# Performance work log

Measured on AMD Instinct MI355X. Metric: run time of the kernel, lower is better.

## Reference

```python
import jax, jax.numpy as jnp
import numpy as np

ATTRACTION_W = 1.0
REPULSION_W = 1.0
MARGIN = 0.3  # hardcoded local `margin = 0.3` in the torch forward


def setup_inputs() -> dict:
    key = jax.random.key(0)
    k1, k2, k3 = jax.random.split(key, 3)
    B, N, D, K = 16, 65536, 32, 512
    beta = jax.random.normal(k1, (B, N, 1), dtype=jnp.float32)
    embed = jax.random.normal(k2, (B, N, D), dtype=jnp.float32)
    # instance id per hit: -1 = background, 0..K-1 = instances
    sid = jax.random.randint(k3, (B, N), -1, K).astype(jnp.int32)
    # first K hits are the condensation points, one per instance
    sid = sid.at[:, :K].set(jnp.arange(K, dtype=jnp.int32)[None, :])
    is_cp = jnp.zeros((B, N), dtype=jnp.int32).at[:, :K].set(1)
    return {"beta": beta, "embed": embed, "slice_id": sid, "is_cp": is_cp, "num_instances": K}


def _per_batch(beta_b, emb_b, sid, iscp, K):
    # beta_b: [N], emb_b: [N, D], sid/iscp: [N]
    N = sid.shape[0]
    cp = iscp == 1
    valid = sid >= 0
    noncp = valid & ~cp  # non-cp signal hits
    pos = cp.sum().astype(jnp.float32)
    neg = jnp.float32(N) - pos  # noncp + background
    pos_w = jax.lax.stop_gradient(neg / (pos + 1e-6))
    w = jnp.where(cp, pos_w, jnp.where(noncp, 1.0, 2.0))
    # weighted BCE-with-logits, reduction='mean'
    x = beta_b
    y = cp.astype(jnp.float32)
    bce = jnp.maximum(x, 0.0) - x * y + jnp.log1p(jnp.exp(-jnp.abs(x)))
    beta_ce = (w * bce).mean()

    # segment id: valid hits -> sid, background -> dummy segment K (dropped)
    seg = jnp.where(valid, sid, K)
    counts = jax.ops.segment_sum(valid.astype(jnp.float32), seg, num_segments=K + 1)[:K]
    inst_exists = counts > 0  # the `unique()` set

    # first cp hit index per instance (sentinel N if instance has no cp)
    idxs = jnp.arange(N)
    first_cp = jax.ops.segment_min(jnp.where(cp & valid, idxs, N), seg, num_segments=K + 1)[:K]
    has_cp = first_cp < N
    safe_cp = jnp.minimum(first_cp, N - 1)
    cp_emb = emb_b[safe_cp]  # [K, D]
    cp_beta = beta_b[safe_cp]  # [K]

    # attraction: sum over instances (with a cp) of mean ||e_hit - e_cp||^2
    sid_c = jnp.clip(sid, 0, K - 1)
    d2 = ((emb_b - cp_emb[sid_c]) ** 2).sum(-1)  # [N]
    d2 = jnp.where(valid, d2, 0.0)
    seg_d2 = jax.ops.segment_sum(d2, seg, num_segments=K + 1)[:K]
    attr = (jnp.where(has_cp & inst_exists, seg_d2 / jnp.maximum(counts, 1.0), 0.0).sum()
            * ATTRACTION_W)

    # ranking: instances with exactly 1 cp and >0 noncp hits
    cp_count = jax.ops.segment_sum((cp & valid).astype(jnp.float32), seg, num_segments=K + 1)[:K]
    ncp_count = jax.ops.segment_sum(noncp.astype(jnp.float32), seg, num_segments=K + 1)[:K]
    r = jax.nn.relu(beta_b + MARGIN - cp_beta[sid_c])
    r = jnp.where(noncp, r, 0.0)
    seg_r = jax.ops.segment_sum(r, seg, num_segments=K + 1)[:K]
    qual = (cp_count == 1.0) & (ncp_count > 0)
    n_unique = inst_exists.sum().astype(jnp.float32)
    ranking = (jnp.where(qual, seg_r / jnp.maximum(ncp_count, 1.0), 0.0).sum()
               / jnp.maximum(n_unique, 1.0))

    beta_loss = beta_ce + 2.0 * ranking

    # repulsion over all cp hits; data has exactly one cp per instance so the
    # cp set equals cp_emb (K points), matching torch's emb_b[cp_idx]
    diff = cp_emb[:, None, :] - cp_emb[None, :, :]  # [K, K, D]
    rep = jnp.exp(-(diff ** 2).sum(-1)).mean() * REPULSION_W

    return beta_loss + attr + rep, beta_loss, attr, rep


def reference(beta, embed, slice_id, is_cp, num_instances):
    K = int(num_instances)
    beta2 = beta[..., 0]  # squeeze(-1)
    loss_b, bl, al, rl = jax.vmap(lambda b, e, s, c: _per_batch(b, e, s, c, K))(
        beta2, embed, slice_id, is_cp)
    return loss_b.mean(), bl.mean(), al.mean(), rl.mean()
```

## Files before the change

kernel.cpp:

```cpp
#include <hip/hip_runtime.h>
#include <math.h>

#define N_HITS 65536
#define K_INST 512
#define MARGIN 0.3f
#define MAXB   16
#define BPB    32
#define HITS_PB (N_HITS / BPB)

__device__ int    g_cnt[MAXB * K_INST];
__device__ float  g_d2v[MAXB * K_INST];
__device__ float  g_rv [MAXB * K_INST];
__device__ int    g_fcp[MAXB * K_INST];
__device__ float  g_cpbeta[MAXB * K_INST];
__device__ float4 g_cpemb[MAXB * K_INST * 8];
__device__ int    g_pcc[MAXB * BPB * K_INST];
__device__ float  g_pcd[MAXB * BPB * K_INST];
__device__ float  g_pcr[MAXB * BPB * K_INST];
__device__ int    g_pos[MAXB];
__device__ float  g_scp[MAXB], g_sncp[MAXB], g_sbg[MAXB];
__device__ float  g_attr[MAXB], g_rank[MAXB], g_nuq[MAXB], g_rep[MAXB];
__device__ int    g_ctr;

__global__ __launch_bounds__(256) void k_init() {
    int i = blockIdx.x * 256 + threadIdx.x;
    if (i < MAXB * K_INST) {
        g_cnt[i] = 0; g_d2v[i] = 0.f; g_rv[i] = 0.f;
        g_fcp[i] = 0x7F7F7F7F;
    }
    if (i < MAXB) {
        g_pos[i] = 0; g_scp[i] = 0.f; g_sncp[i] = 0.f; g_sbg[i] = 0.f;
        g_attr[i] = 0.f; g_rank[i] = 0.f; g_nuq[i] = 0.f; g_rep[i] = 0.f;
    }
    if (i == 0) g_ctr = 0;
}

__global__ __launch_bounds__(256) void k_scan(
    const int* __restrict__ sid, const int* __restrict__ iscp) {
    int b = blockIdx.y;
    size_t bo = (size_t)b * N_HITS;
    int i = blockIdx.x * 256 + threadIdx.x;
    int stride = gridDim.x * 256;
    for (; i < N_HITS; i += stride) {
        int c = iscp[bo + i];
        if (c == 1) {
            atomicAdd(&g_pos[b], 1);
            int s = sid[bo + i];
            if (s >= 0) atomicMin(&g_fcp[b * K_INST + s], i);
        }
    }
}

__global__ __launch_bounds__(256) void k_gather(
    const float* __restrict__ beta, const float4* __restrict__ embed4, int B) {
    int g = blockIdx.x * 256 + threadIdx.x;
    int total = B * K_INST * 8;
    if (g >= total) return;
    int row = g >> 3, sub = g & 7;
    int b = row / K_INST;
    int fc = g_fcp[row];
    int safe = min(fc, N_HITS - 1);
    float4 e = embed4[((size_t)b * N_HITS + safe) * 8 + sub];
    g_cpemb[(size_t)row * 8 + sub] = e;
    if (sub == 0) g_cpbeta[row] = beta[b * N_HITS + safe];
}

__global__ __launch_bounds__(256) void k_bce(
    const float* __restrict__ beta,
    const int* __restrict__ sid_g, const int* __restrict__ iscp_g, int B) {
    __shared__ float l_cb[K_INST];
    __shared__ int   l_cnt[K_INST];
    __shared__ float l_r[K_INST];
    __shared__ float l_red[12];

    int b = blockIdx.y, tid = threadIdx.x;
    size_t bo = (size_t)b * N_HITS;
    int base = blockIdx.x * HITS_PB;

    for (int k = tid; k < K_INST; k += 256) {
        l_cnt[k] = 0; l_r[k] = 0.f;
        l_cb[k] = g_cpbeta[b * K_INST + k];
    }
    __syncthreads();

    float a_cp = 0.f, a_ncp = 0.f, a_bg = 0.f;
    int sv[8], cv[8];
    float xv[8];
#pragma unroll
    for (int i = 0; i < 8; ++i) {
        size_t h = bo + base + i * 256 + tid;
        sv[i] = sid_g[h];
        cv[i] = iscp_g[h];
        xv[i] = beta[h];
    }
#pragma unroll
    for (int i = 0; i < 8; ++i) {
        int s = sv[i];
        bool cp = (cv[i] == 1), valid = (s >= 0), noncp = valid && !cp;
        float x = xv[i];
        float t = __expf(-fabsf(x));
        float bce = fmaxf(x, 0.f) - (cp ? x : 0.f) + __logf(1.f + t);
        if (cp) a_cp += bce; else if (noncp) a_ncp += bce; else a_bg += bce;
        if (valid) {
            atomicAdd(&l_cnt[s], cp ? (1 << 20) : 1);
            if (noncp) {
                float r = x + MARGIN - l_cb[s];
                if (r > 0.f) atomicAdd(&l_r[s], r);
            }
        }
    }

    for (int o = 32; o > 0; o >>= 1) {
        a_cp  += __shfl_down(a_cp, o);
        a_ncp += __shfl_down(a_ncp, o);
        a_bg  += __shfl_down(a_bg, o);
    }
    int wave = tid >> 6;
    if ((tid & 63) == 0) { l_red[wave] = a_cp; l_red[4 + wave] = a_ncp; l_red[8 + wave] = a_bg; }
    __syncthreads();
    if (tid == 0) {
        atomicAdd(&g_scp[b],  l_red[0] + l_red[1] + l_red[2]  + l_red[3]);
        atomicAdd(&g_sncp[b], l_red[4] + l_red[5] + l_red[6]  + l_red[7]);
        atomicAdd(&g_sbg[b],  l_red[8] + l_red[9] + l_red[10] + l_red[11]);
    }
    size_t po = ((size_t)b * BPB + blockIdx.x) * K_INST;
    for (int k = tid; k < K_INST; k += 256) {
        g_pcc[po + k] = l_cnt[k];
        g_pcr[po + k] = l_r[k];
    }
}

__global__ __launch_bounds__(512, 4) void k_d2(
    const float4* __restrict__ embed4,
    const int* __restrict__ sid_g, int B) {
    __shared__ float4 l_cp[K_INST * 8];
    __shared__ float  l_d2[K_INST];

    int b = blockIdx.y, tid = threadIdx.x;
    size_t bo = (size_t)b * N_HITS;
    int base = blockIdx.x * HITS_PB;

    {
        const float4* cpt = g_cpemb + (size_t)b * K_INST * 8;
        for (int idx = tid; idx < K_INST * 8; idx += 512) {
            int k = idx >> 3, j = idx & 7;
            l_cp[(k << 3) | (j ^ (k & 7))] = cpt[idx];
        }
    }
    for (int k = tid; k < K_INST; k += 512) l_d2[k] = 0.f;
    __syncthreads();

    int sub = tid & 7, hgrp = tid >> 3;
#pragma unroll
    for (int g = 0; g < 4; ++g) {
        float4 e[8];
        int sv[8];
#pragma unroll
        for (int k = 0; k < 8; ++k) {
            int hit = base + (g * 8 + k) * 64 + hgrp;
            sv[k] = sid_g[bo + hit];
            e[k]  = embed4[(bo + hit) * 8 + sub];
        }
#pragma unroll
        for (int k = 0; k < 8; ++k) {
            int s = sv[k];
            int row = max(s, 0);
            float4 c4 = l_cp[(row << 3) | (sub ^ (row & 7))];
            float dx = e[k].x - c4.x, dy = e[k].y - c4.y;
            float dz = e[k].z - c4.z, dw = e[k].w - c4.w;
            float q = dx * dx + dy * dy + dz * dz + dw * dw;
            q += __shfl_xor(q, 1);
            q += __shfl_xor(q, 2);
            q += __shfl_xor(q, 4);
            if (sub == 0 && s >= 0) atomicAdd(&l_d2[s], q);
        }
    }

    __syncthreads();
    size_t po = ((size_t)b * BPB + blockIdx.x) * K_INST;
    for (int k = tid; k < K_INST; k += 512) g_pcd[po + k] = l_d2[k];
}

__global__ __launch_bounds__(256) void k_reduce() {
    __shared__ int   rc[4][64];
    __shared__ float rd[4][64];
    __shared__ float rr[4][64];
    int kl = threadIdx.x & 63, p4 = threadIdx.x >> 6;
    int bin = blockIdx.x * 64 + kl;
    int b = bin / K_INST;
    size_t basep = ((size_t)b * BPB) * K_INST + (bin % K_INST);
    int cs = 0; float ds = 0.f, rs = 0.f;
    for (int p = p4 * (BPB / 4); p < (p4 + 1) * (BPB / 4); ++p) {
        cs += g_pcc[basep + (size_t)p * K_INST];
        ds += g_pcd[basep + (size_t)p * K_INST];
        rs += g_pcr[basep + (size_t)p * K_INST];
    }
    rc[p4][kl] = cs; rd[p4][kl] = ds; rr[p4][kl] = rs;
    __syncthreads();
    if (p4 == 0) {
        g_cnt[bin] = rc[0][kl] + rc[1][kl] + rc[2][kl] + rc[3][kl];
        g_d2v[bin] = rd[0][kl] + rd[1][kl] + rd[2][kl] + rd[3][kl];
        g_rv[bin]  = rr[0][kl] + rr[1][kl] + rr[2][kl] + rr[3][kl];
    }
}

__global__ __launch_bounds__(512) void k_tail(float* out, int B) {
    int tid = threadIdx.x;
    int nrep = B * 16;

    if ((int)blockIdx.x < nrep) {
        __shared__ float4 tile[32 * 8];
        __shared__ float red[8];
        int b = blockIdx.x >> 4, t2 = blockIdx.x & 15;
        const float4* base = g_cpemb + (size_t)b * K_INST * 8;
        float4 r0[8];
#pragma unroll
        for (int cc = 0; cc < 8; ++cc) r0[cc] = base[(size_t)tid * 8 + cc];
        if (tid < 256) tile[tid] = base[(size_t)t2 * 256 + tid];
        __syncthreads();
        float acc = 0.f;
        for (int j = 0; j < 32; ++j) {
            float d2 = 0.f;
#pragma unroll
            for (int cc = 0; cc < 8; ++cc) {
                float4 ev = tile[j * 8 + cc];
                float ax = r0[cc].x - ev.x, ay = r0[cc].y - ev.y;
                float az = r0[cc].z - ev.z, aw = r0[cc].w - ev.w;
                d2 += ax * ax + ay * ay + az * az + aw * aw;
            }
            acc += __expf(-d2);
        }
        for (int o = 32; o > 0; o >>= 1) acc += __shfl_down(acc, o);
        if ((tid & 63) == 0) red[tid >> 6] = acc;
        __syncthreads();
        if (tid == 0) {
            float t = 0.f;
            for (int w = 0; w < 8; ++w) t += red[w];
            atomicAdd(&g_rep[b], t);
        }
    } else {
        __shared__ float red2[3][8];
        int b = blockIdx.x - nrep, k = tid;
        int v = g_cnt[b * K_INST + k];
        int ncp = v & 0xFFFFF, cpc = v >> 20;
        int counts = ncp + cpc;
        int fc = g_fcp[b * K_INST + k];
        bool has_cp = fc < N_HITS, exists = counts > 0;
        float segd = g_d2v[b * K_INST + k];
        float attr = (has_cp && exists) ? segd / fmaxf((float)counts, 1.f) : 0.f;
        float rank = (cpc == 1 && ncp > 0) ? g_rv[b * K_INST + k] / fmaxf((float)ncp, 1.f) : 0.f;
        float uq = exists ? 1.f : 0.f;
        for (int o = 32; o > 0; o >>= 1) {
            attr += __shfl_down(attr, o);
            rank += __shfl_down(rank, o);
            uq   += __shfl_down(uq, o);
        }
        if ((k & 63) == 0) { red2[0][k >> 6] = attr; red2[1][k >> 6] = rank; red2[2][k >> 6] = uq; }
        __syncthreads();
        if (k == 0) {
            float a = 0.f, r = 0.f, u = 0.f;
            for (int w = 0; w < 8; ++w) { a += red2[0][w]; r += red2[1][w]; u += red2[2][w]; }
            g_attr[b] = a; g_rank[b] = r; g_nuq[b] = u;
        }
    }

    __shared__ int is_last;
    __syncthreads();
    if (tid == 0) {
        __threadfence();
        int v = atomicAdd(&g_ctr, 1);
        is_last = (v == (int)gridDim.x - 1);
    }
    __syncthreads();
    if (is_last) {
        __threadfence();
        if (tid < 64) {
            int b = tid;
            float loss = 0.f, bl = 0.f, at = 0.f, rp = 0.f;
            if (b < B) {
                float pos = (float)g_pos[b];
                float pw = ((float)N_HITS - pos) / (pos + 1e-6f);
                float bce = (pw * g_scp[b] + g_sncp[b] + 2.f * g_sbg[b]) / (float)N_HITS;
                float rank = g_rank[b] / fmaxf(g_nuq[b], 1.f);
                bl = bce + 2.f * rank;
                at = g_attr[b];
                rp = g_rep[b] / (float)(K_INST * K_INST);
                loss = bl + at + rp;
            }
            for (int o = 32; o > 0; o >>= 1) {
                loss += __shfl_down(loss, o);
                bl   += __shfl_down(bl, o);
                at   += __shfl_down(at, o);
                rp   += __shfl_down(rp, o);
            }
            if (tid == 0) {
                float inv = 1.f / (float)B;
                out[0] = loss * inv;
                out[1] = bl * inv;
                out[2] = at * inv;
                out[3] = rp * inv;
            }
        }
    }
}

extern "C" void kernel_launch(void* const* d_in, const int* in_sizes, int n_in,
                              void* d_out, int out_size, void* d_ws, size_t ws_size,
                              hipStream_t stream) {
    const float*  beta   = (const float*)d_in[0];
    const float*  embed  = (const float*)d_in[1];
    const int*    sid    = (const int*)d_in[2];
    const int*    iscp   = (const int*)d_in[3];
    float* out = (float*)d_out;

    int BN = in_sizes[0];
    int B  = BN / N_HITS;
    if (B > MAXB) B = MAXB;
    int BK = B * K_INST;

    (void)d_ws; (void)ws_size;

    k_init<<<(MAXB * K_INST + 255) / 256, 256, 0, stream>>>();

    k_scan<<<dim3(32, B), 256, 0, stream>>>(sid, iscp);

    k_gather<<<(BK * 8 + 255) / 256, 256, 0, stream>>>(beta, (const float4*)embed, B);

    k_bce<<<dim3(BPB, B), 256, 0, stream>>>(beta, sid, iscp, B);

    k_d2<<<dim3(BPB, B), 512, 0, stream>>>((const float4*)embed, sid, B);

    k_reduce<<<BK / 64, 256, 0, stream>>>();

    k_tail<<<B * 16 + B, 512, 0, stream>>>(out, B);
}
```

Baseline: 251.7 us.

## Stream embeddings into LDS with async global_load_lds ring buffer in k_d2

Rewrites the attraction-distance kernel to use 1024-thread blocks, with 16 blocks per batch instead of 32. Each wave loads its slice ids into LDS, then streams embedding tiles through a 4-deep LDS ring using direct global-to-LDS loads, with vmcnt waits to overlap loads and compute. The partial-sum buffers and the reduce kernel are split so the d2 partials use the new block count. The aim is to hide memory latency on the 128MB embed read, at the cost of more LDS per block, possibly lower occupancy, and reliance on low-level builtins.

```diff
diff --git a/kernel.cpp b/kernel.cpp
--- a/kernel.cpp
+++ b/kernel.cpp
@@ -5,8 +5,10 @@
 #define K_INST 512
 #define MARGIN 0.3f
 #define MAXB   16
-#define BPB    32
-#define HITS_PB (N_HITS / BPB)
+#define BPB_A  32
+#define BPB_D  16
+#define HITS_A (N_HITS / BPB_A)
+#define HITS_D (N_HITS / BPB_D)
 
 __device__ int    g_cnt[MAXB * K_INST];
 __device__ float  g_d2v[MAXB * K_INST];
@@ -14,13 +16,26 @@
 __device__ int    g_fcp[MAXB * K_INST];
 __device__ float  g_cpbeta[MAXB * K_INST];
 __device__ float4 g_cpemb[MAXB * K_INST * 8];
-__device__ int    g_pcc[MAXB * BPB * K_INST];
-__device__ float  g_pcd[MAXB * BPB * K_INST];
-__device__ float  g_pcr[MAXB * BPB * K_INST];
+__device__ int    g_pcc[MAXB * BPB_A * K_INST];
+__device__ float  g_pcr[MAXB * BPB_A * K_INST];
+__device__ float  g_pcd[MAXB * BPB_D * K_INST];
 __device__ int    g_pos[MAXB];
 __device__ float  g_scp[MAXB], g_sncp[MAXB], g_sbg[MAXB];
 __device__ float  g_attr[MAXB], g_rank[MAXB], g_nuq[MAXB], g_rep[MAXB];
 __device__ int    g_ctr;
+
+__device__ __forceinline__ void gl_lds16(const void* g, void* l) {
+    __builtin_amdgcn_global_load_lds(
+        (const __attribute__((address_space(1))) void*)g,
+        (__attribute__((address_space(3))) void*)l, 16, 0, 0);
+}
+__device__ __forceinline__ void gl_lds4(const void* g, void* l) {
+    __builtin_amdgcn_global_load_lds(
+        (const __attribute__((address_space(1))) void*)g,
+        (__attribute__((address_space(3))) void*)l, 4, 0, 0);
+}
+#define WAITV(n) do { asm volatile("s_waitcnt vmcnt(" #n ")" ::: "memory"); \
+                      __builtin_amdgcn_sched_barrier(0); } while (0)
 
 __global__ __launch_bounds__(256) void k_init() {
     int i = blockIdx.x * 256 + threadIdx.x;
@@ -75,7 +90,7 @@
 
     int b = blockIdx.y, tid = threadIdx.x;
     size_t bo = (size_t)b * N_HITS;
-    int base = blockIdx.x * HITS_PB;
+    int base = blockIdx.x * HITS_A;
 
     for (int k = tid; k < K_INST; k += 256) {
         l_cnt[k] = 0; l_r[k] = 0.f;
@@ -123,62 +138,73 @@
         atomicAdd(&g_sncp[b], l_red[4] + l_red[5] + l_red[6]  + l_red[7]);
         atomicAdd(&g_sbg[b],  l_red[8] + l_red[9] + l_red[10] + l_red[11]);
     }
-    size_t po = ((size_t)b * BPB + blockIdx.x) * K_INST;
+    size_t po = ((size_t)b * BPB_A + blockIdx.x) * K_INST;
     for (int k = tid; k < K_INST; k += 256) {
         g_pcc[po + k] = l_cnt[k];
         g_pcr[po + k] = l_r[k];
     }
 }
 
-__global__ __launch_bounds__(512, 4) void k_d2(
-    const float4* __restrict__ embed4,
-    const int* __restrict__ sid_g, int B) {
+__global__ __launch_bounds__(1024, 4) void k_d2(
+    const float4* __restrict__ embed4, const int* __restrict__ sid_g, int B) {
     __shared__ float4 l_cp[K_INST * 8];
+    __shared__ float4 l_tile[16 * 4 * 64];
+    __shared__ int    l_sid[16 * 256];
     __shared__ float  l_d2[K_INST];
 
     int b = blockIdx.y, tid = threadIdx.x;
     size_t bo = (size_t)b * N_HITS;
-    int base = blockIdx.x * HITS_PB;
+    int base = blockIdx.x * HITS_D;
+    int wv = tid >> 6, ln = tid & 63;
+    int wbase = base + wv * 256;
+
+#pragma unroll
+    for (int j = 0; j < 4; ++j)
+        gl_lds4(&sid_g[bo + wbase + j * 64 + ln], &l_sid[(wv << 8) + j * 64]);
+#pragma unroll
+    for (int t = 0; t < 3; ++t)
+        gl_lds16(&embed4[(bo + wbase + t * 8) * 8 + ln],
+                 &l_tile[(wv * 4 + t) * 64]);
 
     {
         const float4* cpt = g_cpemb + (size_t)b * K_INST * 8;
-        for (int idx = tid; idx < K_INST * 8; idx += 512) {
+        for (int idx = tid; idx < K_INST * 8; idx += 1024) {
             int k = idx >> 3, j = idx & 7;
             l_cp[(k << 3) | (j ^ (k & 7))] = cpt[idx];
         }
     }
-    for (int k = tid; k < K_INST; k += 512) l_d2[k] = 0.f;
-    __syncthreads();
-
-    int sub = tid & 7, hgrp = tid >> 3;
-#pragma unroll
-    for (int g = 0; g < 4; ++g) {
-        float4 e[8];
-        int sv[8];
-#pragma unroll
-        for (int k = 0; k < 8; ++k) {
-            int hit = base + (g * 8 + k) * 64 + hgrp;
-            sv[k] = sid_g[bo + hit];
-            e[k]  = embed4[(bo + hit) * 8 + sub];
-        }
-#pragma unroll
-        for (int k = 0; k < 8; ++k) {
-            int s = sv[k];
-            int row = max(s, 0);
-            float4 c4 = l_cp[(row << 3) | (sub ^ (row & 7))];
-            float dx = e[k].x - c4.x, dy = e[k].y - c4.y;
-            float dz = e[k].z - c4.z, dw = e[k].w - c4.w;
-            float q = dx * dx + dy * dy + dz * dz + dw * dw;
-            q += __shfl_xor(q, 1);
-            q += __shfl_xor(q, 2);
-            q += __shfl_xor(q, 4);
-            if (sub == 0 && s >= 0) atomicAdd(&l_d2[s], q);
-        }
-    }
-
-    __syncthreads();
-    size_t po = ((size_t)b * BPB + blockIdx.x) * K_INST;
-    for (int k = tid; k < K_INST; k += 512) g_pcd[po + k] = l_d2[k];
+    for (int k = tid; k < K_INST; k += 1024) l_d2[k] = 0.f;
+    __syncthreads();
+
+    int sub = ln & 7, h8 = ln >> 3;
+    auto consume = [&](int t) {
+        int s = l_sid[(wv << 8) + (t << 3) + h8];
+        float4 e = l_tile[(wv * 4 + (t & 3)) * 64 + ln];
+        int row = max(s, 0);
+        float4 c4 = l_cp[(row << 3) | (sub ^ (row & 7))];
+        float dx = e.x - c4.x, dy = e.y - c4.y;
+        float dz = e.z - c4.z, dw = e.w - c4.w;
+        float q = dx * dx + dy * dy + dz * dz + dw * dw;
+        q += __shfl_xor(q, 1);
+        q += __shfl_xor(q, 2);
+        q += __shfl_xor(q, 4);
+        if (sub == 0 && s >= 0) atomicAdd(&l_d2[s], q);
+    };
+
+#pragma unroll 1
+    for (int t = 0; t < 29; ++t) {
+        WAITV(2);
+        gl_lds16(&embed4[(bo + wbase + (t + 3) * 8) * 8 + ln],
+                 &l_tile[(wv * 4 + ((t + 3) & 3)) * 64]);
+        consume(t);
+    }
+    WAITV(2); consume(29);
+    WAITV(1); consume(30);
+    WAITV(0); consume(31);
+
+    __syncthreads();
+    if (tid < K_INST)
+        g_pcd[((size_t)b * BPB_D + blockIdx.x) * K_INST + tid] = l_d2[tid];
 }
 
 __global__ __launch_bounds__(256) void k_reduce() {
@@ -187,14 +213,16 @@
     __shared__ float rr[4][64];
     int kl = threadIdx.x & 63, p4 = threadIdx.x >> 6;
     int bin = blockIdx.x * 64 + kl;
-    int b = bin / K_INST;
-    size_t basep = ((size_t)b * BPB) * K_INST + (bin % K_INST);
+    int b = bin / K_INST, kk = bin % K_INST;
+    size_t basea = ((size_t)b * BPB_A) * K_INST + kk;
+    size_t based = ((size_t)b * BPB_D) * K_INST + kk;
     int cs = 0; float ds = 0.f, rs = 0.f;
-    for (int p = p4 * (BPB / 4); p < (p4 + 1) * (BPB / 4); ++p) {
-        cs += g_pcc[basep + (size_t)p * K_INST];
-        ds += g_pcd[basep + (size_t)p * K_INST];
-        rs += g_pcr[basep + (size_t)p * K_INST];
-    }
+    for (int p = p4 * 8; p < p4 * 8 + 8; ++p) {
+        cs += g_pcc[basea + (size_t)p * K_INST];
+        rs += g_pcr[basea + (size_t)p * K_INST];
+    }
+    for (int p = p4 * 4; p < p4 * 4 + 4; ++p)
+        ds += g_pcd[based + (size_t)p * K_INST];
     rc[p4][kl] = cs; rd[p4][kl] = ds; rr[p4][kl] = rs;
     __syncthreads();
     if (p4 == 0) {
@@ -326,9 +354,9 @@
 
     k_gather<<<(BK * 8 + 255) / 256, 256, 0, stream>>>(beta, (const float4*)embed, B);
 
-    k_bce<<<dim3(BPB, B), 256, 0, stream>>>(beta, sid, iscp, B);
-
-    k_d2<<<dim3(BPB, B), 512, 0, stream>>>((const float4*)embed, sid, B);
+    k_bce<<<dim3(BPB_A, B), 256, 0, stream>>>(beta, sid, iscp, B);
+
+    k_d2<<<dim3(BPB_D, B), 1024, 0, stream>>>((const float4*)embed, sid, B);
 
     k_reduce<<<BK / 64, 256, 0, stream>>>();
 
```

New measurement: 249.8 us. No clear change (-0.7%).

## Store cp embeddings as bf16 in LDS and use per-lane partial atomics in k_d2

Applied to the files above, without the earlier changes.

The gather kernel now also writes a bf16 copy of the condensation-point embeddings, and k_d2 loads that copy into shared memory, halving its LDS footprint. The shuffle reduction across the 8 sub-lanes is replaced by per-lane shared-memory atomics into a padded [K][9] partial array, which is summed per instance at the end. The hit loop is no longer unrolled across groups, which lowers register pressure. Using bf16 for the centers loses precision in the attraction distances, and the per-lane atomics raise LDS atomic traffic eightfold.

```diff
diff --git a/kernel.cpp b/kernel.cpp
--- a/kernel.cpp
+++ b/kernel.cpp
@@ -8,19 +8,28 @@
 #define BPB    32
 #define HITS_PB (N_HITS / BPB)
 
-__device__ int    g_cnt[MAXB * K_INST];
-__device__ float  g_d2v[MAXB * K_INST];
-__device__ float  g_rv [MAXB * K_INST];
-__device__ int    g_fcp[MAXB * K_INST];
-__device__ float  g_cpbeta[MAXB * K_INST];
-__device__ float4 g_cpemb[MAXB * K_INST * 8];
-__device__ int    g_pcc[MAXB * BPB * K_INST];
-__device__ float  g_pcd[MAXB * BPB * K_INST];
-__device__ float  g_pcr[MAXB * BPB * K_INST];
-__device__ int    g_pos[MAXB];
-__device__ float  g_scp[MAXB], g_sncp[MAXB], g_sbg[MAXB];
-__device__ float  g_attr[MAXB], g_rank[MAXB], g_nuq[MAXB], g_rep[MAXB];
-__device__ int    g_ctr;
+__device__ int     g_cnt[MAXB * K_INST];
+__device__ float   g_d2v[MAXB * K_INST];
+__device__ float   g_rv [MAXB * K_INST];
+__device__ int     g_fcp[MAXB * K_INST];
+__device__ float   g_cpbeta[MAXB * K_INST];
+__device__ float4  g_cpemb[MAXB * K_INST * 8];
+__device__ ushort4 g_cpbf[MAXB * K_INST * 8];
+__device__ int     g_pcc[MAXB * BPB * K_INST];
+__device__ float   g_pcr[MAXB * BPB * K_INST];
+__device__ float   g_pcd[MAXB * BPB * K_INST];
+__device__ int     g_pos[MAXB];
+__device__ float   g_scp[MAXB], g_sncp[MAXB], g_sbg[MAXB];
+__device__ float   g_attr[MAXB], g_rank[MAXB], g_nuq[MAXB], g_rep[MAXB];
+__device__ int     g_ctr;
+
+__device__ __forceinline__ unsigned short f2bf(float f) {
+    unsigned u = __float_as_uint(f);
+    return (unsigned short)((u + 0x7FFFu + ((u >> 16) & 1u)) >> 16);
+}
+__device__ __forceinline__ float bf2f(unsigned short h) {
+    return __uint_as_float(((unsigned)h) << 16);
+}
 
 __global__ __launch_bounds__(256) void k_init() {
     int i = blockIdx.x * 256 + threadIdx.x;
@@ -62,6 +71,9 @@
     int safe = min(fc, N_HITS - 1);
     float4 e = embed4[((size_t)b * N_HITS + safe) * 8 + sub];
     g_cpemb[(size_t)row * 8 + sub] = e;
+    ushort4 h;
+    h.x = f2bf(e.x); h.y = f2bf(e.y); h.z = f2bf(e.z); h.w = f2bf(e.w);
+    g_cpbf[(size_t)row * 8 + sub] = h;
     if (sub == 0) g_cpbeta[row] = beta[b * N_HITS + safe];
 }
 
@@ -131,54 +143,56 @@
 }
 
 __global__ __launch_bounds__(512, 4) void k_d2(
-    const float4* __restrict__ embed4,
-    const int* __restrict__ sid_g, int B) {
-    __shared__ float4 l_cp[K_INST * 8];
-    __shared__ float  l_d2[K_INST];
+    const float4* __restrict__ embed4, const int* __restrict__ sid_g, int B) {
+    __shared__ ushort4 l_cp[K_INST * 9];
+    __shared__ float   l_dp[K_INST * 9];
 
     int b = blockIdx.y, tid = threadIdx.x;
     size_t bo = (size_t)b * N_HITS;
     int base = blockIdx.x * HITS_PB;
 
     {
-        const float4* cpt = g_cpemb + (size_t)b * K_INST * 8;
+        const ushort4* cpt = g_cpbf + (size_t)b * K_INST * 8;
         for (int idx = tid; idx < K_INST * 8; idx += 512) {
             int k = idx >> 3, j = idx & 7;
-            l_cp[(k << 3) | (j ^ (k & 7))] = cpt[idx];
-        }
-    }
-    for (int k = tid; k < K_INST; k += 512) l_d2[k] = 0.f;
+            l_cp[k * 9 + (j ^ (k & 7))] = cpt[idx];
+        }
+    }
+    for (int i = tid; i < K_INST * 9; i += 512) l_dp[i] = 0.f;
     __syncthreads();
 
     int sub = tid & 7, hgrp = tid >> 3;
-#pragma unroll
+#pragma unroll 1
     for (int g = 0; g < 4; ++g) {
+        int sv[8];
         float4 e[8];
-        int sv[8];
-#pragma unroll
-        for (int k = 0; k < 8; ++k) {
-            int hit = base + (g * 8 + k) * 64 + hgrp;
-            sv[k] = sid_g[bo + hit];
-            e[k]  = embed4[(bo + hit) * 8 + sub];
-        }
-#pragma unroll
-        for (int k = 0; k < 8; ++k) {
-            int s = sv[k];
+#pragma unroll
+        for (int j = 0; j < 8; ++j) {
+            int hit = base + (g * 8 + j) * 64 + hgrp;
+            sv[j] = sid_g[bo + hit];
+            e[j]  = embed4[(bo + hit) * 8 + sub];
+        }
+#pragma unroll
+        for (int j = 0; j < 8; ++j) {
+            int s = sv[j];
             int row = max(s, 0);
-            float4 c4 = l_cp[(row << 3) | (sub ^ (row & 7))];
-            float dx = e[k].x - c4.x, dy = e[k].y - c4.y;
-            float dz = e[k].z - c4.z, dw = e[k].w - c4.w;
+            ushort4 h = l_cp[row * 9 + (sub ^ (row & 7))];
+            float c0 = bf2f(h.x), c1 = bf2f(h.y), c2 = bf2f(h.z), c3 = bf2f(h.w);
+            float dx = e[j].x - c0, dy = e[j].y - c1;
+            float dz = e[j].z - c2, dw = e[j].w - c3;
             float q = dx * dx + dy * dy + dz * dz + dw * dw;
-            q += __shfl_xor(q, 1);
-            q += __shfl_xor(q, 2);
-            q += __shfl_xor(q, 4);
-            if (sub == 0 && s >= 0) atomicAdd(&l_d2[s], q);
+            if (s >= 0) atomicAdd(&l_dp[row * 9 + sub], q);
         }
     }
 
     __syncthreads();
     size_t po = ((size_t)b * BPB + blockIdx.x) * K_INST;
-    for (int k = tid; k < K_INST; k += 512) g_pcd[po + k] = l_d2[k];
+    for (int s2 = tid; s2 < K_INST; s2 += 512) {
+        float t = 0.f;
+#pragma unroll
+        for (int u = 0; u < 8; ++u) t += l_dp[s2 * 9 + u];
+        g_pcd[po + s2] = t;
+    }
 }
 
 __global__ __launch_bounds__(256) void k_reduce() {
@@ -187,10 +201,10 @@
     __shared__ float rr[4][64];
     int kl = threadIdx.x & 63, p4 = threadIdx.x >> 6;
     int bin = blockIdx.x * 64 + kl;
-    int b = bin / K_INST;
-    size_t basep = ((size_t)b * BPB) * K_INST + (bin % K_INST);
+    int b = bin / K_INST, kk = bin % K_INST;
+    size_t basep = ((size_t)b * BPB) * K_INST + kk;
     int cs = 0; float ds = 0.f, rs = 0.f;
-    for (int p = p4 * (BPB / 4); p < (p4 + 1) * (BPB / 4); ++p) {
+    for (int p = p4 * 8; p < p4 * 8 + 8; ++p) {
         cs += g_pcc[basep + (size_t)p * K_INST];
         ds += g_pcd[basep + (size_t)p * K_INST];
         rs += g_pcr[basep + (size_t)p * K_INST];
```

Measured after the change: 256.3 us. About the same (+1.9%).
